# Kernel tuning notes

Hardware: AMD Instinct MI355X
Metric: run time of the kernel (lower is better)

The kernel has to match this reference:

```python
import jax, jax.numpy as jnp
import numpy as np

N = 4096      # num_nodes (single graph; batch is all-zeros in the original when absent)
CIN = 1024    # in_channels
H = 1024      # hidden_channels
COUT = 512    # out_channels
R = 10        # nodevec rank (hardcoded in the module)
BN_EPS = 1e-5


def setup_inputs() -> dict:
    key = jax.random.key(0)
    ks = jax.random.split(key, 8)
    w = lambda k, shp: jax.random.normal(k, shp, dtype=jnp.float32) * 0.02
    return {
        "x": jax.random.normal(ks[0], (N, CIN), dtype=jnp.float32),
        "w_map": w(ks[1], (CIN, H)),
        "b_map": jnp.zeros((H,), jnp.float32),
        "nv1": jax.random.normal(ks[2], (N, R), dtype=jnp.float32),
        "nv2": jax.random.normal(ks[3], (R, N), dtype=jnp.float32),
        "w1": w(ks[4], (H, H)),
        "b1": jnp.zeros((H,), jnp.float32),
        "w2": w(ks[5], (H, COUT)),
        "b2": jnp.zeros((COUT,), jnp.float32),
        "bn1_g": jnp.ones((H,), jnp.float32),
        "bn1_b": jnp.zeros((H,), jnp.float32),
        "bn1_m": jnp.zeros((H,), jnp.float32),
        "bn1_v": jnp.ones((H,), jnp.float32),
        "bn2_g": jnp.ones((COUT,), jnp.float32),
        "bn2_b": jnp.zeros((COUT,), jnp.float32),
        "bn2_m": jnp.zeros((COUT,), jnp.float32),
        "bn2_v": jnp.ones((COUT,), jnp.float32),
        "w_attn": w(ks[6], (COUT, 1)),
        "b_attn": jnp.zeros((1,), jnp.float32),
    }


def _batchnorm_eval(h, g, b, m, v):
    # BatchNorm1d in eval mode: running stats
    return (h - m) * jax.lax.rsqrt(v + BN_EPS) * g + b


def reference(x, w_map, b_map, nv1, nv2, w1, b1, w2, b2,
              bn1_g, bn1_b, bn1_m, bn1_v, bn2_g, bn2_b, bn2_m, bn2_v,
              w_attn, b_attn):
    # feature mapping
    xm = jax.nn.relu(x @ w_map + b_map)                       # [N, H]
    # adaptive adjacency: softmax(relu(nv1 @ nv2), dim=1) -> strictly positive,
    # so nonzero() yields the fully dense edge list; we keep it dense.
    adp = jax.nn.softmax(jax.nn.relu(nv1 @ nv2), axis=1)      # [N, N]
    # gcn_norm (PyG GCNConv default): add unit self-loops, normalize by
    # column-degree^-1/2 on both sides.
    A = adp + jnp.eye(N, dtype=adp.dtype)                      # [N, N]
    deg = jnp.sum(A, axis=0)                                   # column sums (target degree)
    dinv = jnp.where(deg > 0, jax.lax.rsqrt(deg), 0.0)
    An = (dinv[:, None] * A) * dinv[None, :]                   # D^-1/2 A D^-1/2
    # GCNConv: out_i = sum_j An[j, i] * (x W)_j + bias  =>  An^T @ (X W) + b
    h = jax.nn.relu(An.T @ (xm @ w1) + b1)                     # conv1 + relu
    h = _batchnorm_eval(h, bn1_g, bn1_b, bn1_m, bn1_v)         # bn1 (dropout off in eval)
    h = jax.nn.relu(An.T @ (h @ w2) + b2)                      # conv2 + relu
    h = _batchnorm_eval(h, bn2_g, bn2_b, bn2_m, bn2_v)         # bn2
    # global_mean_pool with batch == zeros -> single-graph mean
    pooled = jnp.mean(h, axis=0, keepdims=True)                # [1, COUT]
    attn = jax.nn.sigmoid(pooled @ w_attn + b_attn)            # [1, 1]
    return pooled * attn                                       # [1, COUT]
```

## Files before the change

kernel.cpp:

```cpp
#include <hip/hip_runtime.h>

#define NN 4096
#define R_RANK 10

typedef __bf16 bf16x8 __attribute__((ext_vector_type(8)));
typedef float floatx4 __attribute__((ext_vector_type(4)));

__device__ __forceinline__ unsigned short f2bf(float f) {
    union { float f; unsigned int u; } v; v.f = f;
    unsigned int r = v.u + 0x7FFFu + ((v.u >> 16) & 1u);
    return (unsigned short)(r >> 16);
}
__device__ __forceinline__ void gll16(const void* g, void* l) {
    __builtin_amdgcn_global_load_lds(
        (const __attribute__((address_space(1))) unsigned int*)g,
        (__attribute__((address_space(3))) unsigned int*)l, 16, 0, 0);
}
template<int N>
__device__ __forceinline__ void wait_vm() {
    if constexpr (N == 0)       asm volatile("s_waitcnt vmcnt(0)" ::: "memory");
    else if constexpr (N == 3)  asm volatile("s_waitcnt vmcnt(3)" ::: "memory");
    else if constexpr (N == 4)  asm volatile("s_waitcnt vmcnt(4)" ::: "memory");
    else if constexpr (N == 6)  asm volatile("s_waitcnt vmcnt(6)" ::: "memory");
    else if constexpr (N == 8)  asm volatile("s_waitcnt vmcnt(8)" ::: "memory");
    else static_assert(N < 0, "add vmcnt literal");
}
#define SB __builtin_amdgcn_sched_barrier(0)

__global__ __launch_bounds__(256) void row_stats_kernel(
    const float* __restrict__ nv1, const float* __restrict__ nv2,
    float* __restrict__ rowmax, float* __restrict__ rowsum,
    float* __restrict__ deg, float* __restrict__ pooled)
{
    const int i0 = blockIdx.x * 4;
    const int tid = threadIdx.x;
    if (blockIdx.x < 16) deg[blockIdx.x * 256 + tid] = 0.f;
    if (blockIdx.x >= 16 && blockIdx.x < 18) pooled[(blockIdx.x - 16) * 256 + tid] = 0.f;
    __shared__ float a[4][R_RANK];
    if (tid < 4 * R_RANK) a[tid / R_RANK][tid % R_RANK] = nv1[i0 * R_RANK + tid];
    __syncthreads();

    float s[4][16];
    float mx[4] = {0.f, 0.f, 0.f, 0.f};
    #pragma unroll
    for (int t = 0; t < 16; ++t) {
        const int j = t * 256 + tid;
        float v[R_RANK];
        #pragma unroll
        for (int r = 0; r < R_RANK; ++r) v[r] = nv2[r * NN + j];
        #pragma unroll
        for (int q = 0; q < 4; ++q) {
            float acc = 0.f;
            #pragma unroll
            for (int r = 0; r < R_RANK; ++r) acc = fmaf(a[q][r], v[r], acc);
            acc = fmaxf(acc, 0.f);
            s[q][t] = acc;
            mx[q] = fmaxf(mx[q], acc);
        }
    }
    __shared__ float red[4][4];
    #pragma unroll
    for (int q = 0; q < 4; ++q) {
        float m = mx[q];
        #pragma unroll
        for (int off = 32; off > 0; off >>= 1) m = fmaxf(m, __shfl_down(m, off, 64));
        if ((tid & 63) == 0) red[q][tid >> 6] = m;
    }
    __syncthreads();
    #pragma unroll
    for (int q = 0; q < 4; ++q)
        mx[q] = fmaxf(fmaxf(red[q][0], red[q][1]), fmaxf(red[q][2], red[q][3]));
    __syncthreads();
    float sm[4] = {0.f, 0.f, 0.f, 0.f};
    #pragma unroll
    for (int t = 0; t < 16; ++t)
        #pragma unroll
        for (int q = 0; q < 4; ++q) sm[q] += __expf(s[q][t] - mx[q]);
    #pragma unroll
    for (int q = 0; q < 4; ++q) {
        float m = sm[q];
        #pragma unroll
        for (int off = 32; off > 0; off >>= 1) m += __shfl_down(m, off, 64);
        if ((tid & 63) == 0) red[q][tid >> 6] = m;
    }
    __syncthreads();
    if (tid < 4) {
        rowmax[i0 + tid] = mx[tid];
        rowsum[i0 + tid] = red[tid][0] + red[tid][1] + red[tid][2] + red[tid][3];
    }
}

__global__ __launch_bounds__(256) void col_sum_kernel(
    const float* __restrict__ nv1, const float* __restrict__ nv2,
    const float* __restrict__ rowmax, const float* __restrict__ rowsum,
    float* __restrict__ deg)
{
    const int tid = threadIdx.x;
    const int j = blockIdx.x * 256 + tid;
    const int i0 = blockIdx.y * 64;
    __shared__ float a[64][R_RANK];
    __shared__ float rm[64], rs[64];
    if (tid < 64) {
        rm[tid] = rowmax[i0 + tid];
        rs[tid] = 1.0f / rowsum[i0 + tid];
    }
    for (int t = tid; t < 64 * R_RANK; t += 256)
        a[t / R_RANK][t % R_RANK] = nv1[i0 * R_RANK + t];
    __syncthreads();

    float v[R_RANK];
    #pragma unroll
    for (int r = 0; r < R_RANK; ++r) v[r] = nv2[r * NN + j];
    float acc = 0.f;
    #pragma unroll 4
    for (int t = 0; t < 64; ++t) {
        float s = 0.f;
        #pragma unroll
        for (int r = 0; r < R_RANK; ++r) s = fmaf(a[t][r], v[r], s);
        s = fmaxf(s, 0.f);
        acc += __expf(s - rm[t]) * rs[t];
    }
    atomicAdd(&deg[j], acc);
}

__global__ __launch_bounds__(256) void an_build_kernel(
    const float* __restrict__ nv1, const float* __restrict__ nv2,
    const float* __restrict__ rowmax, const float* __restrict__ rowsum,
    const float* __restrict__ deg, unsigned short* __restrict__ AnT)
{
    const int tid = threadIdx.x;
    const int j = blockIdx.x * 256 + tid;
    const int i0 = blockIdx.y * 8;
    __shared__ float v2s[8][R_RANK];
    __shared__ float dis[8];
    if (tid < 8 * R_RANK) {
        const int r = tid / 8, t = tid % 8;
        v2s[t][r] = nv2[r * NN + i0 + t];
    }
    if (tid < 8) dis[tid] = rsqrtf(1.0f + deg[i0 + tid]);

    float a[R_RANK];
    #pragma unroll
    for (int r = 0; r < R_RANK; ++r) a[r] = nv1[j * R_RANK + r];
    const float rm = rowmax[j];
    const float rs = 1.0f / rowsum[j];
    const float dj = rsqrtf(1.0f + deg[j]);
    __syncthreads();

    #pragma unroll
    for (int t = 0; t < 8; ++t) {
        const int i = i0 + t;
        float s = 0.f;
        #pragma unroll
        for (int r = 0; r < R_RANK; ++r) s = fmaf(a[r], v2s[t][r], s);
        s = fmaxf(s, 0.f);
        const float adp = __expf(s - rm) * rs;
        const float val = (adp + ((i == j) ? 1.f : 0.f)) * dis[t] * dj;
        AnT[(size_t)i * NN + j] = f2bf(val);
    }
}

__global__ __launch_bounds__(256) void prep_kernel(
    const float* __restrict__ x, const float* __restrict__ w_map,
    const float* __restrict__ w1, const float* __restrict__ w2,
    unsigned short* __restrict__ xb, unsigned short* __restrict__ wmT,
    unsigned short* __restrict__ w1T, unsigned short* __restrict__ w2T)
{
    const int z = blockIdx.z;
    const int tid = threadIdx.x;
    if (z == 3) {
        const int b = blockIdx.x + blockIdx.y * 32;
        const size_t base = (size_t)b * 4096 + (size_t)tid * 16;
        #pragma unroll
        for (int i = 0; i < 2; ++i) {
            const float4 a0 = *(const float4*)(x + base + i * 8);
            const float4 a1 = *(const float4*)(x + base + i * 8 + 4);
            ushort4 p, q;
            p.x = f2bf(a0.x); p.y = f2bf(a0.y); p.z = f2bf(a0.z); p.w = f2bf(a0.w);
            q.x = f2bf(a1.x); q.y = f2bf(a1.y); q.z = f2bf(a1.z); q.w = f2bf(a1.w);
            *(ushort4*)(xb + base + i * 8) = p;
            *(ushort4*)(xb + base + i * 8 + 4) = q;
        }
        return;
    }
    const float* W = (z == 0) ? w_map : (z == 1) ? w1 : w2;
    unsigned short* WT = (z == 0) ? wmT : (z == 1) ? w1T : w2T;
    const int CN = (z == 2) ? 512 : 1024;
    if (blockIdx.x * 32 >= CN) return;
    __shared__ float s[32][33];
    const int tx = tid & 31, ty = tid >> 5;
    const int r0 = blockIdx.y * 32, c0 = blockIdx.x * 32;
    #pragma unroll
    for (int i = 0; i < 4; ++i)
        s[ty + 8 * i][tx] = W[(size_t)(r0 + ty + 8 * i) * CN + c0 + tx];
    __syncthreads();
    #pragma unroll
    for (int i = 0; i < 4; ++i)
        WT[(size_t)(c0 + ty + 8 * i) * 1024 + r0 + tx] = f2bf(s[tx][ty + 8 * i]);
}

template<int OUTM, int EPI, int SK>
__global__ __launch_bounds__(512) void gemm_mfma(
    const unsigned short* __restrict__ A, const unsigned short* __restrict__ Bt,
    void* __restrict__ Out, const int M, const int N, const int K,
    const float* __restrict__ bias, const float* __restrict__ gamma,
    const float* __restrict__ beta, const float* __restrict__ mean,
    const float* __restrict__ var)
{
    __shared__ __align__(16) unsigned short As[4][8192];
    __shared__ __align__(16) unsigned short Bs[4][8192];
    const int tid = threadIdx.x;
    const int l = tid & 63, w = tid >> 6;
    const int wy = w >> 2, wx = w & 3;
    const int lr = l & 15, lq = l >> 4;

    const int gx = gridDim.x, gy = gridDim.y;
    int lin = blockIdx.x + gx * (blockIdx.y + gy * blockIdx.z);
    const int q = (gx * gy * gridDim.z) >> 3;
    lin = (lin & 7) * q + (lin >> 3);
    const int bx = lin % gx;
    const int by = (lin / gx) % gy;
    const int bz = lin / (gx * gy);

    const int row0 = by * 128, col0 = bx * 128;
    const int Kc = K / SK;
    const int kb = bz * Kc;
    const int nt = Kc >> 6;

    const unsigned short* Ag0 = A + (size_t)(row0 + w * 16 + lr) * K + kb + lq * 8;
    const unsigned short* Bg0 = Bt + (size_t)(col0 + w * 16 + lr) * K + kb + lq * 8;

    floatx4 acc[4][2];
    #pragma unroll
    for (int i = 0; i < 4; ++i)
        #pragma unroll
        for (int j = 0; j < 2; ++j) acc[i][j] = (floatx4){0.f, 0.f, 0.f, 0.f};

    #define STAGE(b, t)                                                         \
    {                                                                           \
        char* Aw = (char*)As[b] + w * 1024;                                     \
        char* Bw = (char*)Bs[b] + w * 1024;                                     \
        const int kk = (t) * 64;                                                \
        gll16(Ag0 + kk,      Aw);                                               \
        gll16(Ag0 + kk + 32, Aw + 8192);                                        \
        gll16(Bg0 + kk,      Bw);                                               \
        gll16(Bg0 + kk + 32, Bw + 8192);                                        \
    }

    STAGE(0, 0)
    STAGE(1, 1)
    for (int t = 0; t < nt; ++t) {
        if (t + 2 < nt) {
            STAGE((t + 2) & 3, t + 2)
            wait_vm<8>();
        } else if (t + 1 < nt) {
            wait_vm<4>();
        } else {
            wait_vm<0>();
        }
        SB; __builtin_amdgcn_s_barrier(); SB;

        const char* Afr = (const char*)As[t & 3] + wy * 4096 + l * 16;
        const char* Bfr = (const char*)Bs[t & 3] + wx * 2048 + l * 16;
        #pragma unroll
        for (int h = 0; h < 2; ++h) {
            bf16x8 af[4], bf[2];
            #pragma unroll
            for (int i = 0; i < 4; ++i) af[i] = *(const bf16x8*)(Afr + h * 8192 + i * 1024);
            #pragma unroll
            for (int j = 0; j < 2; ++j) bf[j] = *(const bf16x8*)(Bfr + h * 8192 + j * 1024);
            #pragma unroll
            for (int mf = 0; mf < 4; ++mf)
                #pragma unroll
                for (int nf = 0; nf < 2; ++nf)
                    acc[mf][nf] = __builtin_amdgcn_mfma_f32_16x16x32_bf16(
                        af[mf], bf[nf], acc[mf][nf], 0, 0, 0);
        }
    }
    #undef STAGE

    const int gr0 = row0 + wy * 64 + lq * 4;
    const int gc0 = col0 + wx * 32 + lr;
    if constexpr (OUTM == 0) {
        float* Pz = (float*)Out + (size_t)bz * M * N;
        #pragma unroll
        for (int mf = 0; mf < 4; ++mf) {
            const int gr = gr0 + mf * 16;
            #pragma unroll
            for (int nf = 0; nf < 2; ++nf) {
                const int gc = gc0 + nf * 16;
                #pragma unroll
                for (int r = 0; r < 4; ++r)
                    Pz[(size_t)(gr + r) * N + gc] = acc[mf][nf][r];
            }
        }
    } else {
        unsigned short* O = (unsigned short*)Out;
        #pragma unroll
        for (int nf = 0; nf < 2; ++nf) {
            const int gc = gc0 + nf * 16;
            float bb = 0.f, sc = 1.f, sh = 0.f;
            if constexpr (EPI >= 1) bb = bias[gc];
            if constexpr (EPI == 2) {
                sc = gamma[gc] * rsqrtf(var[gc] + 1e-5f);
                sh = beta[gc] - mean[gc] * sc;
            }
            #pragma unroll
            for (int mf = 0; mf < 4; ++mf) {
                const int gr = gr0 + mf * 16;
                #pragma unroll
                for (int r = 0; r < 4; ++r) {
                    float xv = acc[mf][nf][r];
                    if constexpr (EPI >= 1) xv = fmaxf(xv + bb, 0.f);
                    if constexpr (EPI == 2) xv = fmaf(xv, sc, sh);
                    O[(size_t)(gr + r) * N + gc] = f2bf(xv);
                }
            }
        }
    }
}

template<int BM, int BN, int SK>
__global__ __launch_bounds__(512, 1) void gemm_big(
    const unsigned short* __restrict__ A, const unsigned short* __restrict__ Bt,
    float* __restrict__ P, const int M, const int N, const int K)
{
    constexpr int MR = BM / 32;
    constexpr int NRF = BN / 64;
    constexpr int NA = BM / 128;
    constexpr int NB = BN / 128;
    constexpr int LPT = NA + NB;
    constexpr int ABYTES = BM * 64;
    __shared__ __align__(16) unsigned short L[4][(BM + BN) * 32];
    const int tid = threadIdx.x;
    const int l = tid & 63, w = tid >> 6;
    const int wy = w >> 2, wx = w & 3;
    const int lr = l & 15, lq = l >> 4;

    const int gx = gridDim.x, gy = gridDim.y;
    int lin = blockIdx.x + gx * (blockIdx.y + gy * blockIdx.z);
    const int q = (gx * gy * gridDim.z) >> 3;
    lin = (lin & 7) * q + (lin >> 3);
    const int bx = lin % gx;
    const int by = (lin / gx) % gy;
    const int bz = lin / (gx * gy);

    const int row0 = by * BM, col0 = bx * BN;
    const int Kc = K / SK, kb = bz * Kc;
    const int nt = Kc >> 5;

    const unsigned short* Ag = A + (size_t)(row0 + w * (BM / 8) + lr) * K + kb + lq * 8;
    const unsigned short* Bg = Bt + (size_t)(col0 + w * (BN / 8) + lr) * K + kb + lq * 8;

    floatx4 acc[MR][NRF];
    #pragma unroll
    for (int i = 0; i < MR; ++i)
        #pragma unroll
        for (int j = 0; j < NRF; ++j) acc[i][j] = (floatx4){0.f, 0.f, 0.f, 0.f};

    #define STAGEB(b, t)                                                        \
    {                                                                           \
        char* Ld = (char*)L[b];                                                 \
        const int kk = (t) * 32;                                                \
        _Pragma("unroll")                                                       \
        for (int s = 0; s < NA; ++s)                                            \
            gll16(Ag + (size_t)(s * 16) * K + kk, Ld + (w * NA + s) * 1024);    \
        _Pragma("unroll")                                                       \
        for (int s = 0; s < NB; ++s)                                            \
            gll16(Bg + (size_t)(s * 16) * K + kk,                               \
                  Ld + ABYTES + (w * NB + s) * 1024);                           \
    }

    STAGEB(0, 0)
    STAGEB(1, 1)
    for (int t = 0; t < nt; ++t) {
        if (t + 2 < nt) {
            STAGEB((t + 2) & 3, t + 2)
            wait_vm<2 * LPT>();
        } else if (t + 1 < nt) {
            wait_vm<LPT>();
        } else {
            wait_vm<0>();
        }
        SB; __builtin_amdgcn_s_barrier(); SB;

        const char* Ab = (const char*)L[t & 3] + wy * (MR * 1024) + l * 16;
        const char* Bb = (const char*)L[t & 3] + ABYTES + wx * (NRF * 1024) + l * 16;
        bf16x8 af[MR], bf[NRF];
        #pragma unroll
        for (int i = 0; i < MR; ++i) af[i] = *(const bf16x8*)(Ab + i * 1024);
        #pragma unroll
        for (int j = 0; j < NRF; ++j) bf[j] = *(const bf16x8*)(Bb + j * 1024);
        __builtin_amdgcn_s_setprio(1);
        #pragma unroll
        for (int mf = 0; mf < MR; ++mf)
            #pragma unroll
            for (int nf = 0; nf < NRF; ++nf)
                acc[mf][nf] = __builtin_amdgcn_mfma_f32_16x16x32_bf16(
                    af[mf], bf[nf], acc[mf][nf], 0, 0, 0);
        __builtin_amdgcn_s_setprio(0);
    }
    #undef STAGEB

    float* Pz = P + (size_t)bz * M * N;
    const int gr0 = row0 + wy * (BM / 2) + lq * 4;
    const int gc0 = col0 + wx * (BN / 4) + lr;
    #pragma unroll
    for (int mf = 0; mf < MR; ++mf) {
        const int gr = gr0 + mf * 16;
        #pragma unroll
        for (int nf = 0; nf < NRF; ++nf) {
            const int gc = gc0 + nf * 16;
            #pragma unroll
            for (int r = 0; r < 4; ++r)
                Pz[(size_t)(gr + r) * N + gc] = acc[mf][nf][r];
        }
    }
}

template<int EPI, int S, int NC>
__global__ __launch_bounds__(256) void reduce_k(
    const float* __restrict__ P, unsigned short* __restrict__ out, const int MN,
    const float* __restrict__ bias, const float* __restrict__ gamma,
    const float* __restrict__ beta, const float* __restrict__ mean,
    const float* __restrict__ var)
{
    const int idx = blockIdx.x * 256 + threadIdx.x;
    const int n4 = MN >> 2;
    const float4* Pv = (const float4*)P;
    float4 v = Pv[idx];
    #pragma unroll
    for (int z = 1; z < S; ++z) {
        const float4 t = Pv[idx + (size_t)z * n4];
        v.x += t.x; v.y += t.y; v.z += t.z; v.w += t.w;
    }
    float vals[4] = {v.x, v.y, v.z, v.w};
    if constexpr (EPI >= 1) {
        const int c0 = (idx << 2) & (NC - 1);
        const float4 b4 = *(const float4*)(bias + c0);
        const float bb[4] = {b4.x, b4.y, b4.z, b4.w};
        float sc[4], sh[4];
        if constexpr (EPI == 2) {
            const float4 g4 = *(const float4*)(gamma + c0);
            const float4 e4 = *(const float4*)(beta + c0);
            const float4 m4 = *(const float4*)(mean + c0);
            const float4 v4 = *(const float4*)(var + c0);
            const float gg[4] = {g4.x, g4.y, g4.z, g4.w};
            const float ee[4] = {e4.x, e4.y, e4.z, e4.w};
            const float mm[4] = {m4.x, m4.y, m4.z, m4.w};
            const float vv[4] = {v4.x, v4.y, v4.z, v4.w};
            #pragma unroll
            for (int j = 0; j < 4; ++j) {
                sc[j] = gg[j] * rsqrtf(vv[j] + 1e-5f);
                sh[j] = ee[j] - mm[j] * sc[j];
            }
        }
        #pragma unroll
        for (int j = 0; j < 4; ++j) {
            float xv = fmaxf(vals[j] + bb[j], 0.f);
            if constexpr (EPI == 2) xv = fmaf(xv, sc[j], sh[j]);
            vals[j] = xv;
        }
    }
    ushort4 p;
    p.x = f2bf(vals[0]); p.y = f2bf(vals[1]); p.z = f2bf(vals[2]); p.w = f2bf(vals[3]);
    *(ushort4*)(out + ((size_t)idx << 2)) = p;
}

template<int S>
__global__ __launch_bounds__(256) void reduce_pool_kernel(
    const float* __restrict__ P, float* __restrict__ pooled,
    const float* __restrict__ bias, const float* __restrict__ gamma,
    const float* __restrict__ beta, const float* __restrict__ mean,
    const float* __restrict__ var)
{
    const int idx = blockIdx.x * 256 + threadIdx.x;
    const int row = blockIdx.x >> 2;
    constexpr int n4 = 512 * 4096 / 4;
    const float4* Pv = (const float4*)P;
    float4 v = Pv[idx];
    #pragma unroll
    for (int z = 1; z < S; ++z) {
        const float4 t = Pv[idx + (size_t)z * n4];
        v.x += t.x; v.y += t.y; v.z += t.z; v.w += t.w;
    }
    const float b0 = bias[row];
    const float sc = gamma[row] * rsqrtf(var[row] + 1e-5f);
    const float sh = beta[row] - mean[row] * sc;
    float s = 0.f;
    const float vals[4] = {v.x, v.y, v.z, v.w};
    #pragma unroll
    for (int j = 0; j < 4; ++j)
        s += fmaf(fmaxf(vals[j] + b0, 0.f), sc, sh);
    #pragma unroll
    for (int off = 32; off > 0; off >>= 1) s += __shfl_down(s, off, 64);
    __shared__ float red[4];
    if ((threadIdx.x & 63) == 0) red[threadIdx.x >> 6] = s;
    __syncthreads();
    if (threadIdx.x == 0)
        atomicAdd(&pooled[row], red[0] + red[1] + red[2] + red[3]);
}

__global__ __launch_bounds__(512) void finalize_kernel(
    const float* __restrict__ pooled, const float* __restrict__ w_attn,
    const float* __restrict__ b_attn, float* __restrict__ out)
{
    const int c = threadIdx.x;
    __shared__ float red[512];
    const float p = pooled[c] * (1.0f / 4096.0f);
    red[c] = p * w_attn[c];
    __syncthreads();
    for (int s = 256; s > 0; s >>= 1) {
        if (c < s) red[c] += red[c + s];
        __syncthreads();
    }
    const float attn = 1.0f / (1.0f + __expf(-(red[0] + b_attn[0])));
    out[c] = p * attn;
}

extern "C" void kernel_launch(void* const* d_in, const int* in_sizes, int n_in,
                              void* d_out, int out_size, void* d_ws, size_t ws_size,
                              hipStream_t stream) {
    const float* x      = (const float*)d_in[0];
    const float* w_map  = (const float*)d_in[1];
    const float* b_map  = (const float*)d_in[2];
    const float* nv1    = (const float*)d_in[3];
    const float* nv2    = (const float*)d_in[4];
    const float* w1     = (const float*)d_in[5];
    const float* b1     = (const float*)d_in[6];
    const float* w2     = (const float*)d_in[7];
    const float* b2     = (const float*)d_in[8];
    const float* bn1_g  = (const float*)d_in[9];
    const float* bn1_b  = (const float*)d_in[10];
    const float* bn1_m  = (const float*)d_in[11];
    const float* bn1_v  = (const float*)d_in[12];
    const float* bn2_g  = (const float*)d_in[13];
    const float* bn2_b  = (const float*)d_in[14];
    const float* bn2_m  = (const float*)d_in[15];
    const float* bn2_v  = (const float*)d_in[16];
    const float* w_attn = (const float*)d_in[17];
    const float* b_attn = (const float*)d_in[18];
    float* out = (float*)d_out;

    const size_t MB = 1024 * 1024;
    const bool big = ws_size >= 118 * MB;
    char* ws = (char*)d_ws;
    unsigned short* AnT = (unsigned short*)(ws);
    float*          P   = (float*)(ws + 32 * MB);
    char* B0 = big ? (ws + 96 * MB) : (ws + 64 * MB);
    unsigned short* xb  = (unsigned short*)(B0);
    unsigned short* t1T = (unsigned short*)(B0);
    unsigned short* t2T = (unsigned short*)(B0);
    unsigned short* xm  = (unsigned short*)(B0 + 8 * MB);
    unsigned short* h1  = (unsigned short*)(B0 + 8 * MB);
    unsigned short* wmT = (unsigned short*)(B0 + 16 * MB);
    unsigned short* w1T = (unsigned short*)(B0 + 18 * MB);
    unsigned short* w2T = (unsigned short*)(B0 + 20 * MB);
    float* deg    = (float*)(B0 + 21 * MB);
    float* rowmax = deg + 4096;
    float* rowsum = rowmax + 4096;
    float* pooled = rowsum + 4096;

    prep_kernel<<<dim3(32, 32, 4), 256, 0, stream>>>(x, w_map, w1, w2, xb, wmT, w1T, w2T);
    row_stats_kernel<<<1024, 256, 0, stream>>>(nv1, nv2, rowmax, rowsum, deg, pooled);
    col_sum_kernel<<<dim3(16, 64), 256, 0, stream>>>(nv1, nv2, rowmax, rowsum, deg);
    an_build_kernel<<<dim3(16, 512), 256, 0, stream>>>(nv1, nv2, rowmax, rowsum, deg, AnT);

    gemm_mfma<1, 1, 1><<<dim3(8, 32, 1), 512, 0, stream>>>(xb, wmT, xm,
        4096, 1024, 1024, b_map, nullptr, nullptr, nullptr, nullptr);
    gemm_mfma<1, 0, 1><<<dim3(32, 8, 1), 512, 0, stream>>>(w1T, xm, t1T,
        1024, 4096, 1024, nullptr, nullptr, nullptr, nullptr, nullptr);
    if (big) {
        gemm_big<256, 256, 4><<<dim3(4, 16, 4), 512, 0, stream>>>(AnT, t1T, P, 4096, 1024, 4096);
        reduce_k<2, 4, 1024><<<4096, 256, 0, stream>>>(P, h1, 4194304,
            b1, bn1_g, bn1_b, bn1_m, bn1_v);
    } else {
        gemm_big<256, 128, 2><<<dim3(8, 16, 2), 512, 0, stream>>>(AnT, t1T, P, 4096, 1024, 4096);
        reduce_k<2, 2, 1024><<<4096, 256, 0, stream>>>(P, h1, 4194304,
            b1, bn1_g, bn1_b, bn1_m, bn1_v);
    }
    gemm_mfma<0, 0, 2><<<dim3(32, 4, 2), 512, 0, stream>>>(w2T, h1, P,
        512, 4096, 1024, nullptr, nullptr, nullptr, nullptr, nullptr);
    reduce_k<0, 2, 1><<<2048, 256, 0, stream>>>(P, t2T, 2097152,
        nullptr, nullptr, nullptr, nullptr, nullptr);
    if (big) {
        gemm_big<256, 256, 8><<<dim3(16, 2, 8), 512, 0, stream>>>(t2T, AnT, P, 512, 4096, 4096);
        reduce_pool_kernel<8><<<2048, 256, 0, stream>>>(
            P, pooled, b2, bn2_g, bn2_b, bn2_m, bn2_v);
    } else {
        gemm_big<256, 128, 4><<<dim3(32, 2, 4), 512, 0, stream>>>(t2T, AnT, P, 512, 4096, 4096);
        reduce_pool_kernel<4><<<2048, 256, 0, stream>>>(
            P, pooled, b2, bn2_g, bn2_b, bn2_m, bn2_v);
    }

    finalize_kernel<<<1, 512, 0, stream>>>(pooled, w_attn, b_attn, out);
}
```

Baseline: 294.1 us.

## Replace big split-K GEMMs with 128x128-tile multi-block-occupancy kernel

Adds a new split-K GEMM kernel that uses 128x128 tiles, 256 threads and launch bounds allowing four blocks per CU, with a simple single-buffered LDS load per 64-wide K step and an XCD-aware block remapping. The two large An-transpose GEMMs in the 'big' path switch from the 256x256 pipelined kernel to it. The goal is to hide latency through occupancy rather than explicit multi-stage buffering and to spread work across more blocks. The trade-off is lower per-tile data reuse and a sync between load and compute each iteration.

```diff
diff --git a/kernel.cpp b/kernel.cpp
--- a/kernel.cpp
+++ b/kernel.cpp
@@ -316,6 +316,91 @@
                     O[(size_t)(gr + r) * N + gc] = f2bf(xv);
                 }
             }
+        }
+    }
+}
+
+template<int SK>
+__global__ __launch_bounds__(256, 4) void gemm97(
+    const unsigned short* __restrict__ A, const unsigned short* __restrict__ Bt,
+    float* __restrict__ P, const int M, const int N, const int K)
+{
+    __shared__ __align__(16) unsigned short As[8192];
+    __shared__ __align__(16) unsigned short Bs[8192];
+    const int tid = threadIdx.x;
+    const int l = tid & 63, w = tid >> 6;
+    const int wy = w >> 1, wx = w & 1;
+    const int lr = l & 15, lq = l >> 4;
+
+    const int gx = gridDim.x, gy = gridDim.y;
+    int lin = blockIdx.x + gx * (blockIdx.y + gy * blockIdx.z);
+    const int q = (gx * gy * gridDim.z) >> 3;
+    lin = (lin & 7) * q + (lin >> 3);
+    const int bx = lin % gx;
+    const int by = (lin / gx) % gy;
+    const int bz = lin / (gx * gy);
+
+    const int row0 = by * 128, col0 = bx * 128;
+    const int Kc = K / SK;
+    const int kb = bz * Kc;
+    const int nt = Kc >> 6;
+
+    const unsigned short* Ag0 = A + (size_t)(row0 + 2 * w * 16 + lr) * K + kb + lq * 8;
+    const unsigned short* Ag1 = Ag0 + (size_t)16 * K;
+    const unsigned short* Bg0 = Bt + (size_t)(col0 + 2 * w * 16 + lr) * K + kb + lq * 8;
+    const unsigned short* Bg1 = Bg0 + (size_t)16 * K;
+    char* Asw = (char*)As + 2 * w * 1024;
+    char* Bsw = (char*)Bs + 2 * w * 1024;
+
+    floatx4 acc[4][4];
+    #pragma unroll
+    for (int i = 0; i < 4; ++i)
+        #pragma unroll
+        for (int j = 0; j < 4; ++j) acc[i][j] = (floatx4){0.f, 0.f, 0.f, 0.f};
+
+    const char* Afr = (const char*)As + wy * 4096 + l * 16;
+    const char* Bfr = (const char*)Bs + wx * 4096 + l * 16;
+
+    for (int t = 0; t < nt; ++t) {
+        const int k0 = t * 64;
+        __syncthreads();
+        #pragma unroll
+        for (int h = 0; h < 2; ++h) {
+            gll16(Ag0 + k0 + h * 32, Asw + h * 8192);
+            gll16(Ag1 + k0 + h * 32, Asw + h * 8192 + 1024);
+            gll16(Bg0 + k0 + h * 32, Bsw + h * 8192);
+            gll16(Bg1 + k0 + h * 32, Bsw + h * 8192 + 1024);
+        }
+        __syncthreads();
+
+        #pragma unroll
+        for (int h = 0; h < 2; ++h) {
+            bf16x8 af[4], bf[4];
+            #pragma unroll
+            for (int i = 0; i < 4; ++i) af[i] = *(const bf16x8*)(Afr + h * 8192 + i * 1024);
+            #pragma unroll
+            for (int i = 0; i < 4; ++i) bf[i] = *(const bf16x8*)(Bfr + h * 8192 + i * 1024);
+            #pragma unroll
+            for (int mf = 0; mf < 4; ++mf)
+                #pragma unroll
+                for (int nf = 0; nf < 4; ++nf)
+                    acc[mf][nf] = __builtin_amdgcn_mfma_f32_16x16x32_bf16(
+                        af[mf], bf[nf], acc[mf][nf], 0, 0, 0);
+        }
+    }
+
+    float* Pz = P + (size_t)bz * M * N;
+    const int gr0 = row0 + wy * 64 + lq * 4;
+    const int gc0 = col0 + wx * 64 + lr;
+    #pragma unroll
+    for (int mf = 0; mf < 4; ++mf) {
+        const int gr = gr0 + mf * 16;
+        #pragma unroll
+        for (int nf = 0; nf < 4; ++nf) {
+            const int gc = gc0 + nf * 16;
+            #pragma unroll
+            for (int r = 0; r < 4; ++r)
+                Pz[(size_t)(gr + r) * N + gc] = acc[mf][nf][r];
         }
     }
 }
@@ -571,7 +656,7 @@
     gemm_mfma<1, 0, 1><<<dim3(32, 8, 1), 512, 0, stream>>>(w1T, xm, t1T,
         1024, 4096, 1024, nullptr, nullptr, nullptr, nullptr, nullptr);
     if (big) {
-        gemm_big<256, 256, 4><<<dim3(4, 16, 4), 512, 0, stream>>>(AnT, t1T, P, 4096, 1024, 4096);
+        gemm97<4><<<dim3(8, 32, 4), 256, 0, stream>>>(AnT, t1T, P, 4096, 1024, 4096);
         reduce_k<2, 4, 1024><<<4096, 256, 0, stream>>>(P, h1, 4194304,
             b1, bn1_g, bn1_b, bn1_m, bn1_v);
     } else {
@@ -584,7 +669,7 @@
     reduce_k<0, 2, 1><<<2048, 256, 0, stream>>>(P, t2T, 2097152,
         nullptr, nullptr, nullptr, nullptr, nullptr);
     if (big) {
-        gemm_big<256, 256, 8><<<dim3(16, 2, 8), 512, 0, stream>>>(t2T, AnT, P, 512, 4096, 4096);
+        gemm97<8><<<dim3(32, 4, 8), 256, 0, stream>>>(t2T, AnT, P, 512, 4096, 4096);
         reduce_pool_kernel<8><<<2048, 256, 0, stream>>>(
             P, pooled, b2, bn2_g, bn2_b, bn2_m, bn2_v);
     } else {
```

After: 337.3 us. 1.15x slower.
